# Optimization experiments

Hardware: AMD Instinct MI355X
Metric: run time of the kernel (lower is better)

## Reference

```python
import jax, jax.numpy as jnp
import numpy as np

HEADS = 8
DIM_HEAD = 64
NUM_MEM_KV = 4

def rmsnorm(x, g):
    # F.normalize(x, dim=1) * g * sqrt(C): L2-normalize over channel dim with eps clamp
    n = jnp.sqrt(jnp.sum(x * x, axis=1, keepdims=True))
    return x / jnp.maximum(n, 1e-12) * g * (x.shape[1] ** 0.5)

def setup_inputs() -> dict:
    key = jax.random.key(0)
    ks = jax.random.split(key, 7)
    b, c, h, w = 32, 512, 32, 32
    hidden = HEADS * DIM_HEAD
    x = jax.random.normal(ks[0], (b, c, h, w), jnp.float32)
    g_in = 1.0 + 0.02 * jax.random.normal(ks[1], (1, c, 1, 1), jnp.float32)
    w_qkv = jax.random.normal(ks[2], (3 * hidden, c), jnp.float32) * (c ** -0.5)
    mem_kv = jax.random.normal(ks[3], (2, HEADS, DIM_HEAD, NUM_MEM_KV), jnp.float32)
    w_out = jax.random.normal(ks[4], (c, hidden), jnp.float32) * (hidden ** -0.5)
    b_out = 0.01 * jax.random.normal(ks[5], (c,), jnp.float32)
    g_out = 1.0 + 0.02 * jax.random.normal(ks[6], (1, c, 1, 1), jnp.float32)
    return {"x": x, "g_in": g_in, "w_qkv": w_qkv, "mem_kv": mem_kv,
            "w_out": w_out, "b_out": b_out, "g_out": g_out}

def reference(x, g_in, w_qkv, mem_kv, w_out, b_out, g_out):
    b, c, h, w = x.shape
    scale = DIM_HEAD ** -0.5
    xn = rmsnorm(x, g_in)
    # 1x1 conv (no bias) == channel GEMM
    qkv = jnp.einsum('bchw,oc->bohw', xn, w_qkv)
    q, k, v = jnp.split(qkv, 3, axis=1)
    to_heads = lambda t: t.reshape(b, HEADS, DIM_HEAD, h * w)  # b (h c) x y -> b h c (xy)
    q, k, v = map(to_heads, (q, k, v))
    mk = jnp.broadcast_to(mem_kv[0], (b,) + mem_kv[0].shape)
    mv = jnp.broadcast_to(mem_kv[1], (b,) + mem_kv[1].shape)
    k = jnp.concatenate([mk, k], axis=-1)
    v = jnp.concatenate([mv, v], axis=-1)
    q = jax.nn.softmax(q, axis=-2) * scale   # softmax over feature dim d
    k = jax.nn.softmax(k, axis=-1)           # softmax over sequence dim n
    context = jnp.einsum('bhdn,bhen->bhde', k, v)
    out = jnp.einsum('bhde,bhdn->bhen', context, q)
    out = out.reshape(b, HEADS * DIM_HEAD, h, w)
    out = jnp.einsum('bchw,oc->bohw', out, w_out) + b_out[None, :, None, None]
    return rmsnorm(out, g_out)
```

## Files before the change

kernel.cpp:

```cpp
#include <hip/hip_runtime.h>
#include <hip/hip_bf16.h>


#define AS1 __attribute__((address_space(1)))
#define AS3 __attribute__((address_space(3)))

using short8 = __attribute__((ext_vector_type(8))) short;
using usht4  = __attribute__((ext_vector_type(4))) unsigned short;
using f32x4  = __attribute__((ext_vector_type(4))) float;

__device__ __forceinline__ unsigned short f2bf(float f) {
  unsigned int u = __float_as_uint(f);
  u += 0x7fffu + ((u >> 16) & 1u);
  return (unsigned short)(u >> 16);
}
__device__ __forceinline__ float bf2f(unsigned short s) {
  return __uint_as_float(((unsigned int)s) << 16);
}

__global__ __launch_bounds__(256, 4)
void norm_r(const float* __restrict__ X, float* __restrict__ R) {
  __shared__ float part[32][33];
  const int t = threadIdx.x;
  const int b = blockIdx.x >> 5;
  const int pos0 = (blockIdx.x & 31) * 32;
  const int pg = t & 7, cg = t >> 3;
  const float* xp = X + ((size_t)b * 512 + (size_t)cg * 16) * 1024 + pos0 + pg * 4;
  f32x4 s = {0.f, 0.f, 0.f, 0.f};
#pragma unroll
  for (int i = 0; i < 16; ++i) {
    f32x4 v = *(const f32x4*)(xp + (size_t)i * 1024);
    s += v * v;
  }
  part[cg][pg * 4 + 0] = s.x;
  part[cg][pg * 4 + 1] = s.y;
  part[cg][pg * 4 + 2] = s.z;
  part[cg][pg * 4 + 3] = s.w;
  __syncthreads();
  if (t < 32) {
    float tot = 0.f;
#pragma unroll
    for (int j = 0; j < 32; ++j) tot += part[j][t];
    R[(size_t)b * 1024 + pos0 + t] = 22.627416998f / fmaxf(sqrtf(tot), 1e-12f);
  }
}

__global__ __launch_bounds__(256, 4)
void norm_r_bf16(const unsigned short* __restrict__ X, float* __restrict__ R) {
  __shared__ float part[16][64];
  const int t = threadIdx.x;
  const int b = blockIdx.x >> 4;
  const int pos0 = (blockIdx.x & 15) * 64;
  const int pg = t & 15, cg = t >> 4;
  const unsigned short* xp =
      X + ((size_t)b * 512 + (size_t)cg * 32) * 1024 + pos0 + pg * 4;
  float s0 = 0.f, s1 = 0.f, s2 = 0.f, s3 = 0.f;
#pragma unroll 8
  for (int i = 0; i < 32; ++i) {
    usht4 v = *(const usht4*)(xp + (size_t)i * 1024);
    float a = bf2f(v.x), bb = bf2f(v.y), c = bf2f(v.z), d = bf2f(v.w);
    s0 += a * a; s1 += bb * bb; s2 += c * c; s3 += d * d;
  }
  part[cg][pg * 4 + 0] = s0;
  part[cg][pg * 4 + 1] = s1;
  part[cg][pg * 4 + 2] = s2;
  part[cg][pg * 4 + 3] = s3;
  __syncthreads();
  if (t < 64) {
    float tot = 0.f;
#pragma unroll
    for (int j = 0; j < 16; ++j) tot += part[j][t];
    R[(size_t)b * 1024 + pos0 + t] = 22.627416998f / fmaxf(sqrtf(tot), 1e-12f);
  }
}

__global__ __launch_bounds__(256, 4)
void xn_transpose(const float* __restrict__ X, const float* __restrict__ R,
                  unsigned short* __restrict__ XT) {
  __shared__ float tile[64][65];
  const int t = threadIdx.x;
  const int b = blockIdx.z, cb = blockIdx.y, pb = blockIdx.x;
  {
    const int p = t & 63, cg = t >> 6;
    const float r = R[(size_t)b * 1024 + pb * 64 + p];
    const float* xp = X + ((size_t)b * 512 + (size_t)(cb * 64 + cg * 16)) * 1024 + pb * 64 + p;
#pragma unroll
    for (int i = 0; i < 16; ++i)
      tile[cg * 16 + i][p] = xp[(size_t)i * 1024] * r;
  }
  __syncthreads();
#pragma unroll
  for (int k = 0; k < 2; ++k) {
    const int idx = k * 256 + t;
    const int p = idx >> 3, c8 = idx & 7;
    short8 v;
#pragma unroll
    for (int j = 0; j < 8; ++j) v[j] = (short)f2bf(tile[c8 * 8 + j][p]);
    *(short8*)(XT + ((size_t)b * 1024 + pb * 64 + p) * 512 + cb * 64 + c8 * 8) = v;
  }
}

__global__ __launch_bounds__(256, 4)
void cast_wqkv(const float* __restrict__ W, const float* __restrict__ g,
               unsigned short* __restrict__ O) {
  int i = blockIdx.x * 256 + threadIdx.x;
  O[i] = f2bf(W[i] * g[i & 511]);
}
__global__ __launch_bounds__(256, 4)
void cast_w(const float* __restrict__ W, unsigned short* __restrict__ O, int n) {
  int i = blockIdx.x * 256 + threadIdx.x;
  if (i < n) O[i] = f2bf(W[i]);
}

template <int MTOT, bool SPLIT3, bool BIAS>
__global__ __launch_bounds__(256, 2)
void gemm_bt(const unsigned short* __restrict__ A,
             const unsigned short* __restrict__ Ball,
             unsigned short* __restrict__ O0, unsigned short* __restrict__ O1,
             unsigned short* __restrict__ O2, const float* __restrict__ bias) {
  __shared__ char smem[34816];
  unsigned short* lA = (unsigned short*)smem;
  unsigned short* lB = lA + 128 * 64;
  const int t = threadIdx.x;
  const int lane = t & 63, w = t >> 6;
  const int wm = w >> 1, wn = w & 1;
  const int mt = blockIdx.x >> 3, nt = blockIdx.x & 7;
  const int b = blockIdx.y;
  const unsigned short* Ag = A + (size_t)(mt * 128) * 512;
  const unsigned short* Bg = Ball + ((size_t)b * 1024 + (size_t)nt * 128) * 512;
  const int scol = ((lane & 7) ^ (lane >> 3)) * 8;
  f32x4 acc[4][4] = {};

  for (int kt = 0; kt < 8; ++kt) {
    const unsigned short* As = Ag + kt * 64 + scol;
    const unsigned short* Bs = Bg + kt * 64 + scol;
#pragma unroll
    for (int i = 0; i < 4; ++i) {
      const int r = w * 32 + i * 8 + (lane >> 3);
      __builtin_amdgcn_global_load_lds(
          (const AS1 unsigned int*)(As + (size_t)r * 512),
          (AS3 unsigned int*)(lA + (w * 32 + i * 8) * 64), 16, 0, 0);
      __builtin_amdgcn_global_load_lds(
          (const AS1 unsigned int*)(Bs + (size_t)r * 512),
          (AS3 unsigned int*)(lB + (w * 32 + i * 8) * 64), 16, 0, 0);
    }
    __syncthreads();
#pragma unroll
    for (int ks = 0; ks < 2; ++ks) {
      const int pch = ((ks * 4 + (lane >> 4)) ^ (lane & 7)) * 8;
      short8 af[4], bfv[4];
#pragma unroll
      for (int i = 0; i < 4; ++i)
        af[i] = *(const short8*)(lA + (wm * 64 + i * 16 + (lane & 15)) * 64 + pch);
#pragma unroll
      for (int j = 0; j < 4; ++j)
        bfv[j] = *(const short8*)(lB + (wn * 64 + j * 16 + (lane & 15)) * 64 + pch);
#pragma unroll
      for (int i = 0; i < 4; ++i)
#pragma unroll
        for (int j = 0; j < 4; ++j)
          acc[i][j] = __builtin_amdgcn_mfma_f32_16x16x32_bf16(af[i], bfv[j],
                                                              acc[i][j], 0, 0, 0);
    }
    __syncthreads();
  }

  unsigned short* Cst = (unsigned short*)smem;
#pragma unroll
  for (int i = 0; i < 4; ++i)
#pragma unroll
    for (int j = 0; j < 4; ++j)
#pragma unroll
      for (int r = 0; r < 4; ++r) {
        const int row = wm * 64 + i * 16 + (lane >> 4) * 4 + r;
        const int col = wn * 64 + j * 16 + (lane & 15);
        float v = acc[i][j][r];
        if (BIAS) v += bias[mt * 128 + row];
        Cst[row * 136 + col] = f2bf(v);
      }
  __syncthreads();
  unsigned short* Og;
  if (SPLIT3) {
    const int sec = mt >> 2;
    unsigned short* base = (sec == 0) ? O0 : ((sec == 1) ? O1 : O2);
    Og = base + ((size_t)b * 512 + (size_t)(mt & 3) * 128) * 1024 + (size_t)nt * 128;
  } else {
    Og = O0 + ((size_t)b * MTOT + (size_t)mt * 128) * 1024 + (size_t)nt * 128;
  }
#pragma unroll
  for (int k = 0; k < 8; ++k) {
    const int f = t + k * 256;
    const int row = f >> 4, c8 = f & 15;
    short8 v = *(const short8*)(Cst + row * 136 + c8 * 8);
    *(short8*)(Og + (size_t)row * 1024 + c8 * 8) = v;
  }
}

__global__ __launch_bounds__(256, 2)
void attn_kernel(const unsigned short* __restrict__ Qp,
                 const unsigned short* __restrict__ Kp,
                 const unsigned short* __restrict__ Vp,
                 const float* __restrict__ memkv,
                 unsigned short* __restrict__ outT) {
  __shared__ char smem[36608];
  unsigned short* bufA = (unsigned short*)smem;
  unsigned short* bufB = (unsigned short*)(smem + 9216);
  float* Pl   = (float*)(smem + 18432);
  float* Pc   = (float*)(smem + 18432);
  float* csS  = (float*)(smem + 21504);
  float* msum = (float*)(smem + 35072);
  float* rsI  = (float*)(smem + 36096);
  const int t = threadIdx.x;
  const int lane = t & 63, wave = t >> 6;
  const int b = blockIdx.x >> 3, h = blockIdx.x & 7;
  const size_t hb = ((size_t)b * 512 + (size_t)h * 64) * 1024;
  const unsigned short* Qg = Qp + hb;
  const unsigned short* Kg = Kp + hb;
  const unsigned short* Vg = Vp + hb;
  const float* mk = memkv + (size_t)h * 256;
  const float* mv = memkv + 2048 + (size_t)h * 256;

  float rsum[2] = {0.f, 0.f};
  f32x4 cacc[4] = {};

  for (int it = 0; it < 17; ++it) {
    if (it == 0) {
      const int d = t & 63, j = t >> 6;
      const float ev = __expf(mk[d * 4 + j]);
      msum[d * 4 + j] = ev;
      bufA[d * 72 + j] = f2bf(ev);
      bufB[d * 72 + j] = f2bf(mv[d * 4 + j]);
      for (int c2 = 4 + j; c2 < 64; c2 += 4) {
        bufA[d * 72 + c2] = 0;
        bufB[d * 72 + c2] = 0;
      }
    } else {
      const int c0 = (it - 1) * 64;
#pragma unroll
      for (int z = 0; z < 2; ++z) {
        const int d = z * 32 + (t >> 3), ch = t & 7;
        short8 kv = *(const short8*)(Kg + (size_t)d * 1024 + c0 + ch * 8);
        short8 pk;
        float ssum = 0.f;
#pragma unroll
        for (int j = 0; j < 8; ++j) {
          const float e = __expf(bf2f((unsigned short)kv[j]));
          ssum += e;
          pk[j] = (short)f2bf(e);
        }
        rsum[z] += ssum;
        *(short8*)(bufA + d * 72 + ch * 8) = pk;
        short8 vv = *(const short8*)(Vg + (size_t)d * 1024 + c0 + ch * 8);
        *(short8*)(bufB + d * 72 + ch * 8) = vv;
      }
    }
    __syncthreads();
#pragma unroll
    for (int ks = 0; ks < 2; ++ks) {
      short8 a = *(const short8*)(bufA + (wave * 16 + (lane & 15)) * 72 +
                                  ks * 32 + (lane >> 4) * 8);
#pragma unroll
      for (int et = 0; et < 4; ++et) {
        short8 bb = *(const short8*)(bufB + (et * 16 + (lane & 15)) * 72 +
                                     ks * 32 + (lane >> 4) * 8);
        cacc[et] = __builtin_amdgcn_mfma_f32_16x16x32_bf16(a, bb, cacc[et], 0, 0, 0);
      }
    }
    __syncthreads();
  }

  Pl[t]       = rsum[0];
  Pl[256 + t] = rsum[1];
  __syncthreads();
  if (t < 64) {
    float s = 0.f;
#pragma unroll
    for (int ch = 0; ch < 8; ++ch) s += Pl[t * 8 + ch];
    s += msum[t * 4] + msum[t * 4 + 1] + msum[t * 4 + 2] + msum[t * 4 + 3];
    rsI[t] = 1.0f / s;
  }
  __syncthreads();

  unsigned short* CT = bufB;
#pragma unroll
  for (int et = 0; et < 4; ++et)
#pragma unroll
    for (int r = 0; r < 4; ++r) {
      const int d = wave * 16 + (lane >> 4) * 4 + r;
      const int e = et * 16 + (lane & 15);
      CT[e * 72 + d] = f2bf(cacc[et][r] * rsI[d]);
    }
  __syncthreads();

  short8 a0 = *(const short8*)(CT + (wave * 16 + (lane & 15)) * 72 + (lane >> 4) * 8);
  short8 a1 = *(const short8*)(CT + (wave * 16 + (lane & 15)) * 72 + 32 + (lane >> 4) * 8);
  unsigned short* oBase = outT + (size_t)b * 1024 * 512 + h * 64;

  for (int pt = 0; pt < 16; ++pt) {
    {
      const int p = lane, dq = wave;
      float cp = 0.f;
#pragma unroll
      for (int i2 = 0; i2 < 8; ++i2) {
        const int d0 = dq * 16 + i2 * 2;
        const float e0 = __expf(bf2f(Qg[(size_t)d0 * 1024 + pt * 64 + p]));
        const float e1 = __expf(bf2f(Qg[(size_t)(d0 + 1) * 1024 + pt * 64 + p]));
        cp += e0 + e1;
        const unsigned int pk =
            (unsigned int)f2bf(e0) | ((unsigned int)f2bf(e1) << 16);
        *(unsigned int*)(bufA + p * 72 + d0) = pk;
      }
      Pc[dq * 64 + p] = cp;
    }
    __syncthreads();
    if (t < 64) csS[t] = 0.125f / (Pc[t] + Pc[64 + t] + Pc[128 + t] + Pc[192 + t]);
    __syncthreads();
#pragma unroll
    for (int ps = 0; ps < 4; ++ps) {
      f32x4 oc = {};
      short8 b0 = *(const short8*)(bufA + (ps * 16 + (lane & 15)) * 72 + (lane >> 4) * 8);
      short8 b1 = *(const short8*)(bufA + (ps * 16 + (lane & 15)) * 72 + 32 + (lane >> 4) * 8);
      oc = __builtin_amdgcn_mfma_f32_16x16x32_bf16(a0, b0, oc, 0, 0, 0);
      oc = __builtin_amdgcn_mfma_f32_16x16x32_bf16(a1, b1, oc, 0, 0, 0);
      const float cs = csS[ps * 16 + (lane & 15)];
      const unsigned long long pk =
          (unsigned long long)f2bf(oc[0] * cs) |
          ((unsigned long long)f2bf(oc[1] * cs) << 16) |
          ((unsigned long long)f2bf(oc[2] * cs) << 32) |
          ((unsigned long long)f2bf(oc[3] * cs) << 48);
      const int p = pt * 64 + ps * 16 + (lane & 15);
      *(unsigned long long*)(oBase + (size_t)p * 512 + wave * 16 + (lane >> 4) * 4) = pk;
    }
    __syncthreads();
  }
}

__global__ __launch_bounds__(256, 4)
void final_scale_bf16(const unsigned short* __restrict__ P,
                      const float* __restrict__ R, const float* __restrict__ G,
                      float* __restrict__ O) {
  const size_t f = ((size_t)blockIdx.x * 256 + threadIdx.x) * 4;
  const int p = (int)(f & 1023);
  const int c = (int)((f >> 10) & 511);
  const int b = (int)(f >> 19);
  usht4 v = *(const usht4*)(P + f);
  const f32x4 r = *(const f32x4*)(R + (size_t)b * 1024 + p);
  const float g = G[c];
  f32x4 o;
  o.x = bf2f(v.x) * r.x * g;
  o.y = bf2f(v.y) * r.y * g;
  o.z = bf2f(v.z) * r.z * g;
  o.w = bf2f(v.w) * r.w * g;
  *(f32x4*)(O + f) = o;
}

extern "C" void kernel_launch(void* const* d_in, const int* in_sizes, int n_in,
                              void* d_out, int out_size, void* d_ws, size_t ws_size,
                              hipStream_t stream) {
  (void)in_sizes; (void)n_in; (void)out_size; (void)ws_size;
  const float* x     = (const float*)d_in[0];
  const float* g_in  = (const float*)d_in[1];
  const float* w_qkv = (const float*)d_in[2];
  const float* memkv = (const float*)d_in[3];
  const float* w_out = (const float*)d_in[4];
  const float* b_out = (const float*)d_in[5];
  const float* g_out = (const float*)d_in[6];
  float* out = (float*)d_out;

  char* ws = (char*)d_ws;
  float* r1           = (float*)ws;
  float* r2           = (float*)(ws + 131072);
  unsigned short* wqb = (unsigned short*)(ws + 262144);
  unsigned short* wob = (unsigned short*)(ws + 1835008);
  unsigned short* xnT = (unsigned short*)(ws + 2359296);
  unsigned short* Qp  = (unsigned short*)(ws + 35913728);
  unsigned short* outT = xnT;
  unsigned short* pre  = Qp;
  unsigned short* Kp  = (unsigned short*)d_out;
  unsigned short* Vp  = (unsigned short*)d_out + 16777216;

  norm_r<<<1024, 256, 0, stream>>>(x, r1);
  xn_transpose<<<dim3(16, 8, 32), 256, 0, stream>>>(x, r1, xnT);
  cast_wqkv<<<3072, 256, 0, stream>>>(w_qkv, g_in, wqb);
  cast_w<<<1024, 256, 0, stream>>>(w_out, wob, 262144);
  gemm_bt<1536, true, false><<<dim3(96, 32), 256, 0, stream>>>(
      wqb, xnT, Qp, Kp, Vp, nullptr);
  attn_kernel<<<256, 256, 0, stream>>>(Qp, Kp, Vp, memkv, outT);
  gemm_bt<512, false, true><<<dim3(32, 32), 256, 0, stream>>>(
      wob, outT, pre, nullptr, nullptr, b_out);
  norm_r_bf16<<<512, 256, 0, stream>>>(pre, r2);
  final_scale_bf16<<<16384, 256, 0, stream>>>(pre, r2, g_out, out);
}
```

Baseline: 277.9 us.

## Fuse RMS norm with transpose/scale, split attention into context and output kernels

Merges the input norm-reduction kernel into the normalize-transpose kernel, so each block computes its own row scales and then transposes all 8 channel tiles. It does the same for the output side, fusing the bf16 norm reduction with the final scale. The single 256-block attention kernel is split into a context kernel and a 1024-block output kernel, which raises parallelism for the Q-side pass. This removes launches and intermediate R buffers but rereads X/pre and adds a global round trip for the context matrices.

Result: no change. 282.6 us (+1.7%).

```diff
diff --git a/kernel.cpp b/kernel.cpp
--- a/kernel.cpp
+++ b/kernel.cpp
@@ -19,84 +19,50 @@
 }
 
 __global__ __launch_bounds__(256, 4)
-void norm_r(const float* __restrict__ X, float* __restrict__ R) {
-  __shared__ float part[32][33];
+void rms_t(const float* __restrict__ X, unsigned short* __restrict__ XT) {
+  __shared__ float partA[16][64];
+  __shared__ float rS[64];
+  __shared__ float tile[64][65];
   const int t = threadIdx.x;
-  const int b = blockIdx.x >> 5;
-  const int pos0 = (blockIdx.x & 31) * 32;
-  const int pg = t & 7, cg = t >> 3;
-  const float* xp = X + ((size_t)b * 512 + (size_t)cg * 16) * 1024 + pos0 + pg * 4;
-  f32x4 s = {0.f, 0.f, 0.f, 0.f};
-#pragma unroll
-  for (int i = 0; i < 16; ++i) {
-    f32x4 v = *(const f32x4*)(xp + (size_t)i * 1024);
-    s += v * v;
-  }
-  part[cg][pg * 4 + 0] = s.x;
-  part[cg][pg * 4 + 1] = s.y;
-  part[cg][pg * 4 + 2] = s.z;
-  part[cg][pg * 4 + 3] = s.w;
-  __syncthreads();
-  if (t < 32) {
-    float tot = 0.f;
-#pragma unroll
-    for (int j = 0; j < 32; ++j) tot += part[j][t];
-    R[(size_t)b * 1024 + pos0 + t] = 22.627416998f / fmaxf(sqrtf(tot), 1e-12f);
-  }
-}
-
-__global__ __launch_bounds__(256, 4)
-void norm_r_bf16(const unsigned short* __restrict__ X, float* __restrict__ R) {
-  __shared__ float part[16][64];
-  const int t = threadIdx.x;
-  const int b = blockIdx.x >> 4;
-  const int pos0 = (blockIdx.x & 15) * 64;
-  const int pg = t & 15, cg = t >> 4;
-  const unsigned short* xp =
-      X + ((size_t)b * 512 + (size_t)cg * 32) * 1024 + pos0 + pg * 4;
-  float s0 = 0.f, s1 = 0.f, s2 = 0.f, s3 = 0.f;
-#pragma unroll 8
-  for (int i = 0; i < 32; ++i) {
-    usht4 v = *(const usht4*)(xp + (size_t)i * 1024);
-    float a = bf2f(v.x), bb = bf2f(v.y), c = bf2f(v.z), d = bf2f(v.w);
-    s0 += a * a; s1 += bb * bb; s2 += c * c; s3 += d * d;
-  }
-  part[cg][pg * 4 + 0] = s0;
-  part[cg][pg * 4 + 1] = s1;
-  part[cg][pg * 4 + 2] = s2;
-  part[cg][pg * 4 + 3] = s3;
+  const int b = blockIdx.y, pb = blockIdx.x;
+  const int pos0 = pb * 64;
+  {
+    const int pg = t & 15, cq = t >> 4;
+    const float* xp = X + ((size_t)b * 512 + (size_t)cq * 32) * 1024 + pos0 + pg * 4;
+    f32x4 s = {0.f, 0.f, 0.f, 0.f};
+#pragma unroll
+    for (int i = 0; i < 32; ++i) {
+      f32x4 v = *(const f32x4*)(xp + (size_t)i * 1024);
+      s += v * v;
+    }
+    *(f32x4*)(&partA[cq][pg * 4]) = s;
+  }
   __syncthreads();
   if (t < 64) {
     float tot = 0.f;
 #pragma unroll
-    for (int j = 0; j < 16; ++j) tot += part[j][t];
-    R[(size_t)b * 1024 + pos0 + t] = 22.627416998f / fmaxf(sqrtf(tot), 1e-12f);
-  }
-}
-
-__global__ __launch_bounds__(256, 4)
-void xn_transpose(const float* __restrict__ X, const float* __restrict__ R,
-                  unsigned short* __restrict__ XT) {
-  __shared__ float tile[64][65];
-  const int t = threadIdx.x;
-  const int b = blockIdx.z, cb = blockIdx.y, pb = blockIdx.x;
-  {
-    const int p = t & 63, cg = t >> 6;
-    const float r = R[(size_t)b * 1024 + pb * 64 + p];
-    const float* xp = X + ((size_t)b * 512 + (size_t)(cb * 64 + cg * 16)) * 1024 + pb * 64 + p;
+    for (int j = 0; j < 16; ++j) tot += partA[j][t];
+    rS[t] = 22.627416998f / fmaxf(sqrtf(tot), 1e-12f);
+  }
+  __syncthreads();
+  const int p = t & 63, cg = t >> 6;
+  const float r = rS[p];
+  for (int cb = 0; cb < 8; ++cb) {
+    const float* xp = X + ((size_t)b * 512 + (size_t)(cb * 64 + cg * 16)) * 1024 + pos0 + p;
 #pragma unroll
     for (int i = 0; i < 16; ++i)
       tile[cg * 16 + i][p] = xp[(size_t)i * 1024] * r;
-  }
-  __syncthreads();
-#pragma unroll
-  for (int k = 0; k < 2; ++k) {
-    const int idx = k * 256 + t;
-    const int p = idx >> 3, c8 = idx & 7;
-    short8 v;
-#pragma unroll
-    for (int j = 0; j < 8; ++j) v[j] = (short)f2bf(tile[c8 * 8 + j][p]);
-    *(short8*)(XT + ((size_t)b * 1024 + pb * 64 + p) * 512 + cb * 64 + c8 * 8) = v;
+    __syncthreads();
+#pragma unroll
+    for (int k = 0; k < 2; ++k) {
+      const int idx = k * 256 + t;
+      const int p2 = idx >> 3, c8 = idx & 7;
+      short8 v;
+#pragma unroll
+      for (int j = 0; j < 8; ++j) v[j] = (short)f2bf(tile[c8 * 8 + j][p2]);
+      *(short8*)(XT + ((size_t)b * 1024 + pos0 + p2) * 512 + cb * 64 + c8 * 8) = v;
+    }
+    __syncthreads();
   }
 }
 
@@ -197,24 +163,19 @@
 }
 
 __global__ __launch_bounds__(256, 2)
-void attn_kernel(const unsigned short* __restrict__ Qp,
-                 const unsigned short* __restrict__ Kp,
-                 const unsigned short* __restrict__ Vp,
-                 const float* __restrict__ memkv,
-                 unsigned short* __restrict__ outT) {
-  __shared__ char smem[36608];
-  unsigned short* bufA = (unsigned short*)smem;
-  unsigned short* bufB = (unsigned short*)(smem + 9216);
-  float* Pl   = (float*)(smem + 18432);
-  float* Pc   = (float*)(smem + 18432);
-  float* csS  = (float*)(smem + 21504);
-  float* msum = (float*)(smem + 35072);
-  float* rsI  = (float*)(smem + 36096);
+void attn_ctx(const unsigned short* __restrict__ Kp,
+              const unsigned short* __restrict__ Vp,
+              const float* __restrict__ memkv,
+              unsigned short* __restrict__ CTg) {
+  __shared__ unsigned short bufA[64 * 72];
+  __shared__ unsigned short bufB[64 * 72];
+  __shared__ float Pl[512];
+  __shared__ float msum[256];
+  __shared__ float rsI[64];
   const int t = threadIdx.x;
   const int lane = t & 63, wave = t >> 6;
   const int b = blockIdx.x >> 3, h = blockIdx.x & 7;
   const size_t hb = ((size_t)b * 512 + (size_t)h * 64) * 1024;
-  const unsigned short* Qg = Qp + hb;
   const unsigned short* Kg = Kp + hb;
   const unsigned short* Vg = Vp + hb;
   const float* mk = memkv + (size_t)h * 256;
@@ -291,12 +252,36 @@
       CT[e * 72 + d] = f2bf(cacc[et][r] * rsI[d]);
     }
   __syncthreads();
-
-  short8 a0 = *(const short8*)(CT + (wave * 16 + (lane & 15)) * 72 + (lane >> 4) * 8);
-  short8 a1 = *(const short8*)(CT + (wave * 16 + (lane & 15)) * 72 + 32 + (lane >> 4) * 8);
+#pragma unroll
+  for (int k2 = 0; k2 < 2; ++k2) {
+    const int idx = k2 * 256 + t;
+    const int e = idx >> 3, ch = idx & 7;
+    short8 v = *(const short8*)(CT + e * 72 + ch * 8);
+    *(short8*)(CTg + (size_t)blockIdx.x * 4096 + e * 64 + ch * 8) = v;
+  }
+}
+
+__global__ __launch_bounds__(256, 4)
+void attn_out(const unsigned short* __restrict__ Qp,
+              const unsigned short* __restrict__ CTg,
+              unsigned short* __restrict__ outT) {
+  __shared__ unsigned short bufA[64 * 72];
+  __shared__ float Pc[256];
+  __shared__ float csS[64];
+  const int t = threadIdx.x;
+  const int lane = t & 63, wave = t >> 6;
+  const int bh = blockIdx.x >> 2, ptq = blockIdx.x & 3;
+  const int b = bh >> 3, h = bh & 7;
+  const unsigned short* Qg = Qp + ((size_t)b * 512 + (size_t)h * 64) * 1024;
+
+  short8 a0 = *(const short8*)(CTg + (size_t)bh * 4096 +
+                               (wave * 16 + (lane & 15)) * 64 + (lane >> 4) * 8);
+  short8 a1 = *(const short8*)(CTg + (size_t)bh * 4096 +
+                               (wave * 16 + (lane & 15)) * 64 + 32 + (lane >> 4) * 8);
   unsigned short* oBase = outT + (size_t)b * 1024 * 512 + h * 64;
 
-  for (int pt = 0; pt < 16; ++pt) {
+  for (int it = 0; it < 4; ++it) {
+    const int pt = ptq * 4 + it;
     {
       const int p = lane, dq = wave;
       float cp = 0.f;
@@ -336,22 +321,50 @@
 }
 
 __global__ __launch_bounds__(256, 4)
-void final_scale_bf16(const unsigned short* __restrict__ P,
-                      const float* __restrict__ R, const float* __restrict__ G,
-                      float* __restrict__ O) {
-  const size_t f = ((size_t)blockIdx.x * 256 + threadIdx.x) * 4;
-  const int p = (int)(f & 1023);
-  const int c = (int)((f >> 10) & 511);
-  const int b = (int)(f >> 19);
-  usht4 v = *(const usht4*)(P + f);
-  const f32x4 r = *(const f32x4*)(R + (size_t)b * 1024 + p);
-  const float g = G[c];
-  f32x4 o;
-  o.x = bf2f(v.x) * r.x * g;
-  o.y = bf2f(v.y) * r.y * g;
-  o.z = bf2f(v.z) * r.z * g;
-  o.w = bf2f(v.w) * r.w * g;
-  *(f32x4*)(O + f) = o;
+void rms_final(const unsigned short* __restrict__ P,
+               const float* __restrict__ G, float* __restrict__ O) {
+  __shared__ float partA[16][64];
+  __shared__ float rS[64];
+  const int t = threadIdx.x;
+  const int b = blockIdx.y, pos0 = blockIdx.x * 64;
+  const int pg = t & 15, cg = t >> 4;
+  const unsigned short* xp =
+      P + ((size_t)b * 512 + (size_t)cg * 32) * 1024 + pos0 + pg * 4;
+  {
+    float s0 = 0.f, s1 = 0.f, s2 = 0.f, s3 = 0.f;
+#pragma unroll
+    for (int i = 0; i < 32; ++i) {
+      usht4 v = *(const usht4*)(xp + (size_t)i * 1024);
+      float a = bf2f(v.x), bb = bf2f(v.y), c = bf2f(v.z), d = bf2f(v.w);
+      s0 += a * a; s1 += bb * bb; s2 += c * c; s3 += d * d;
+    }
+    partA[cg][pg * 4 + 0] = s0;
+    partA[cg][pg * 4 + 1] = s1;
+    partA[cg][pg * 4 + 2] = s2;
+    partA[cg][pg * 4 + 3] = s3;
+  }
+  __syncthreads();
+  if (t < 64) {
+    float tot = 0.f;
+#pragma unroll
+    for (int j = 0; j < 16; ++j) tot += partA[j][t];
+    rS[t] = 22.627416998f / fmaxf(sqrtf(tot), 1e-12f);
+  }
+  __syncthreads();
+  const float r0 = rS[pg * 4], r1 = rS[pg * 4 + 1], r2 = rS[pg * 4 + 2],
+              r3 = rS[pg * 4 + 3];
+  float* op = O + ((size_t)b * 512 + (size_t)cg * 32) * 1024 + pos0 + pg * 4;
+#pragma unroll
+  for (int i = 0; i < 32; ++i) {
+    usht4 v = *(const usht4*)(xp + (size_t)i * 1024);
+    const float g = G[cg * 32 + i];
+    f32x4 o;
+    o.x = bf2f(v.x) * r0 * g;
+    o.y = bf2f(v.y) * r1 * g;
+    o.z = bf2f(v.z) * r2 * g;
+    o.w = bf2f(v.w) * r3 * g;
+    *(f32x4*)(op + (size_t)i * 1024) = o;
+  }
 }
 
 extern "C" void kernel_launch(void* const* d_in, const int* in_sizes, int n_in,
@@ -368,26 +381,24 @@
   float* out = (float*)d_out;
 
   char* ws = (char*)d_ws;
-  float* r1           = (float*)ws;
-  float* r2           = (float*)(ws + 131072);
-  unsigned short* wqb = (unsigned short*)(ws + 262144);
-  unsigned short* wob = (unsigned short*)(ws + 1835008);
-  unsigned short* xnT = (unsigned short*)(ws + 2359296);
-  unsigned short* Qp  = (unsigned short*)(ws + 35913728);
-  unsigned short* outT = xnT;
-  unsigned short* pre  = Qp;
-  unsigned short* Kp  = (unsigned short*)d_out;
-  unsigned short* Vp  = (unsigned short*)d_out + 16777216;
-
-  norm_r<<<1024, 256, 0, stream>>>(x, r1);
-  xn_transpose<<<dim3(16, 8, 32), 256, 0, stream>>>(x, r1, xnT);
+  unsigned short* wob = (unsigned short*)ws;
+  unsigned short* wqb = (unsigned short*)(ws + 524288);
+  unsigned short* xnT = (unsigned short*)(ws + 2097152);
+  unsigned short* CTg = xnT;
+  unsigned short* Qp  = (unsigned short*)(ws + 35651584);
+  unsigned short* pre = Qp;
+  unsigned short* Kp   = (unsigned short*)d_out;
+  unsigned short* Vp   = (unsigned short*)d_out + 16777216;
+  unsigned short* outT = (unsigned short*)d_out;
+
+  rms_t<<<dim3(16, 32), 256, 0, stream>>>(x, xnT);
   cast_wqkv<<<3072, 256, 0, stream>>>(w_qkv, g_in, wqb);
   cast_w<<<1024, 256, 0, stream>>>(w_out, wob, 262144);
   gemm_bt<1536, true, false><<<dim3(96, 32), 256, 0, stream>>>(
       wqb, xnT, Qp, Kp, Vp, nullptr);
-  attn_kernel<<<256, 256, 0, stream>>>(Qp, Kp, Vp, memkv, outT);
+  attn_ctx<<<256, 256, 0, stream>>>(Kp, Vp, memkv, CTg);
+  attn_out<<<1024, 256, 0, stream>>>(Qp, CTg, outT);
   gemm_bt<512, false, true><<<dim3(32, 32), 256, 0, stream>>>(
       wob, outT, pre, nullptr, nullptr, b_out);
-  norm_r_bf16<<<512, 256, 0, stream>>>(pre, r2);
-  final_scale_bf16<<<16384, 256, 0, stream>>>(pre, r2, g_out, out);
-}
+  rms_final<<<dim3(16, 32), 256, 0, stream>>>(pre, g_out, out);
+}
```
